# Kernel tuning notes

Hardware: AMD Instinct MI355X
Metric: run time of the kernel (lower is better)

Reference implementation:

```python
import jax, jax.numpy as jnp
import numpy as np

B, S, D, H = 4, 2048, 1024, 16
HD = D // H  # head dim = 64
NEG = jnp.finfo(jnp.float32).min


def setup_inputs() -> dict:
    key = jax.random.key(0)
    ks = jax.random.split(key, 6)
    states = jax.random.normal(ks[0], (B, S, D), dtype=jnp.float32)
    # causal float mask, broadcastable over batch and heads
    mask = jnp.tril(jnp.ones((S, S), dtype=jnp.float32))[None, None, :, :]
    scale = 1.0 / np.sqrt(D)
    Wq = jax.random.normal(ks[1], (D, D), dtype=jnp.float32) * scale
    Wk = jax.random.normal(ks[2], (D, D), dtype=jnp.float32) * scale
    Wv = jax.random.normal(ks[3], (D, D), dtype=jnp.float32) * scale
    Wo = jax.random.normal(ks[4], (D, D), dtype=jnp.float32) * scale
    return {"states": states, "mask": mask, "Wq": Wq, "Wk": Wk, "Wv": Wv, "Wo": Wo}


def _split_heads(x):
    # [B,S,D] -> [B,H,S,HD]
    return x.reshape(B, S, H, HD).transpose(0, 2, 1, 3)


def reference(states, mask, Wq, Wk, Wv, Wo):
    q = _split_heads(states @ Wq)
    k = _split_heads(states @ Wk)
    v = _split_heads(states @ Wv)
    # scores [B,H,S,S], scaled by rsqrt(head_dim) as in the original
    alpha = jnp.einsum("bhqd,bhkd->bhqk", q, k) * (1.0 / jnp.sqrt(jnp.float32(HD)))
    alpha = alpha * mask + (1.0 - mask) * NEG
    alpha = jax.nn.softmax(alpha, axis=-1)
    ctx = jnp.einsum("bhqk,bhkd->bhqd", alpha, v)
    ctx = ctx.transpose(0, 2, 1, 3).reshape(B, S, D)  # concat heads
    return ctx @ Wo
```

## Files before the change

### kernel.cpp

```cpp
#include <hip/hip_runtime.h>
#include <hip/hip_bf16.h>

#define BB 4
#define SS 2048
#define DD 1024
#define HH 16
#define HDD 64
#define MM (BB*SS)

typedef __attribute__((ext_vector_type(8))) short short8;
typedef __attribute__((ext_vector_type(4))) float f32x4;
typedef __attribute__((ext_vector_type(4))) int int4v;
typedef __attribute__((ext_vector_type(4))) short bf16x4;

__device__ __forceinline__ ushort f2bf(float f) {
  union { float f; uint u; } v; v.f = f;
  uint u = v.u;
  uint r = (u + 0x7FFFu + ((u >> 16) & 1u)) >> 16;
  return (ushort)r;
}

__device__ __forceinline__ float exp2f_fast(float x) {
#if __has_builtin(__builtin_amdgcn_exp2f)
  return __builtin_amdgcn_exp2f(x);
#else
  float r; asm("v_exp_f32 %0, %1" : "=v"(r) : "v"(x)); return r;
#endif
}

__device__ __forceinline__ bf16x4 pack4bf(float a, float b, float c, float d) {
  union { __hip_bfloat162 h2[2]; bf16x4 s; } u;
  u.h2[0] = __float22bfloat162_rn(make_float2(a, b));
  u.h2[1] = __float22bfloat162_rn(make_float2(c, d));
  return u.s;
}

__device__ __forceinline__ f32x4 mfma16(bf16x4 a, bf16x4 b, f32x4 c) {
#if __has_builtin(__builtin_amdgcn_mfma_f32_16x16x16bf16_1k)
  return __builtin_amdgcn_mfma_f32_16x16x16bf16_1k(a, b, c, 0, 0, 0);
#else
  f32x4 d;
  asm volatile("s_nop 1\n\tv_mfma_f32_16x16x16_bf16 %0, %1, %2, %3\n\ts_nop 7\n\ts_nop 3"
               : "=v"(d) : "v"(a), "v"(b), "v"(c));
  return d;
#endif
}

__device__ __forceinline__ void gload16(void* lds, const void* g) {
  __builtin_amdgcn_global_load_lds((const __attribute__((address_space(1))) void*)g,
                                   (__attribute__((address_space(3))) void*)lds, 16, 0, 0);
}

__global__ __launch_bounds__(256) void k_convert(const float* __restrict__ in,
                                                 ushort* __restrict__ out, int n4) {
  int i = blockIdx.x * 256 + threadIdx.x;
  if (i >= n4) return;
  float4 v = ((const float4*)in)[i];
  uint lo = (uint)f2bf(v.x) | ((uint)f2bf(v.y) << 16);
  uint hi = (uint)f2bf(v.z) | ((uint)f2bf(v.w) << 16);
  ((uint2*)out)[i] = make_uint2(lo, hi);
}

__global__ __launch_bounds__(256) void k_transpose(const float* __restrict__ W0, const float* __restrict__ W1,
                                                   const float* __restrict__ W2, const float* __restrict__ W3,
                                                   ushort* __restrict__ T0, ushort* __restrict__ T1,
                                                   ushort* __restrict__ T2, ushort* __restrict__ T3) {
  __shared__ float t[32][33];
  const float* W; ushort* T;
  switch (blockIdx.z) {
    case 0: W = W0; T = T0; break;
    case 1: W = W1; T = T1; break;
    case 2: W = W2; T = T2; break;
    default: W = W3; T = T3; break;
  }
  float scale = (blockIdx.z == 0) ? 0.18033688011112042f : 1.0f;
  int tx = threadIdx.x, ty = threadIdx.y;
  int x = blockIdx.x * 32 + tx;
  int y0 = blockIdx.y * 32;
#pragma unroll
  for (int j = 0; j < 32; j += 8) t[ty + j][tx] = W[(y0 + ty + j) * DD + x];
  __syncthreads();
#pragma unroll
  for (int j = 0; j < 32; j += 8)
    T[(blockIdx.x * 32 + ty + j) * DD + y0 + tx] = f2bf(t[tx][ty + j] * scale);
}

__global__ __launch_bounds__(256) void k_vtrans(const ushort* __restrict__ V,
                                                ushort* __restrict__ Vt) {
  __shared__ ushort t[64][72];
  int bh = blockIdx.y;
  int s0 = blockIdx.x * 64;
  int tid = threadIdx.x;
  int r = tid >> 3, c8 = (tid & 7) * 8;
  const ushort* vp = V + (size_t)bh * SS * HDD;
#pragma unroll
  for (int p = 0; p < 2; p++) {
    int row = r + p * 32;
    *(int4v*)&t[row][c8] = *(const int4v*)(vp + (size_t)(s0 + row) * HDD + c8);
  }
  __syncthreads();
  int hd = tid >> 2, sc = (tid & 3) * 16;
  ushort tmp[16];
#pragma unroll
  for (int j = 0; j < 16; j++) tmp[j] = t[sc + j][hd];
  ushort* op = Vt + ((size_t)bh * HDD + hd) * SS + s0 + sc;
  *(int4v*)op = *(int4v*)tmp;
  *(int4v*)(op + 8) = *(int4v*)(tmp + 8);
}

__device__ __forceinline__ void gemm_tile(const ushort* __restrict__ Arow,
                                          const ushort* __restrict__ Brow,
                                          ushort* Al, ushort* Bl,
                                          f32x4 acc[4][4]) {
  int tid = threadIdx.x;
  int lane = tid & 63, w = tid >> 6;
  int wm = w >> 1, wn = w & 1;
  int lrow = lane & 15, lgrp = lane >> 4;
#pragma unroll
  for (int i = 0; i < 4; i++)
#pragma unroll
    for (int j = 0; j < 4; j++)
#pragma unroll
      for (int r = 0; r < 4; r++) acc[i][j][r] = 0.f;

  int srow = lane >> 2;
  int scolb = (lane & 3) * 16;
  const char* A8 = (const char*)Arow;
  const char* B8 = (const char*)Brow;

#pragma unroll
  for (int ii = 0; ii < 2; ii++) {
    int i = w * 2 + ii;
    gload16(Al + i * 512, A8 + (size_t)(i * 16 + srow) * (DD * 2) + scolb);
    gload16(Bl + i * 512, B8 + (size_t)(i * 16 + srow) * (DD * 2) + scolb);
  }
  __syncthreads();

  for (int kk = 0; kk < DD; kk += 32) {
    int cur = (kk >> 5) & 1;
    if (kk + 32 < DD) {
#pragma unroll
      for (int ii = 0; ii < 2; ii++) {
        int i = w * 2 + ii;
        gload16(Al + (cur ^ 1) * 4096 + i * 512,
                A8 + (size_t)(i * 16 + srow) * (DD * 2) + (kk + 32) * 2 + scolb);
        gload16(Bl + (cur ^ 1) * 4096 + i * 512,
                B8 + (size_t)(i * 16 + srow) * (DD * 2) + (kk + 32) * 2 + scolb);
      }
    }
    short8 a[4], b[4];
#pragma unroll
    for (int i = 0; i < 4; i++) a[i] = *(const short8*)&Al[cur * 4096 + (wm * 64 + i * 16 + lrow) * 32 + lgrp * 8];
#pragma unroll
    for (int j = 0; j < 4; j++) b[j] = *(const short8*)&Bl[cur * 4096 + (wn * 64 + j * 16 + lrow) * 32 + lgrp * 8];
#pragma unroll
    for (int i = 0; i < 4; i++)
#pragma unroll
      for (int j = 0; j < 4; j++)
        acc[i][j] = __builtin_amdgcn_mfma_f32_16x16x32_bf16(a[i], b[j], acc[i][j], 0, 0, 0);
    __syncthreads();
  }
}

__global__ __launch_bounds__(256) void k_qkv(const ushort* __restrict__ X,
                                             const ushort* __restrict__ Wqt,
                                             const ushort* __restrict__ Wkt,
                                             const ushort* __restrict__ Wvt,
                                             ushort* __restrict__ Q,
                                             ushort* __restrict__ K,
                                             ushort* __restrict__ V) {
  __shared__ ushort Al[2 * 4096];
  __shared__ ushort Bl[2 * 4096];
  const ushort* Wt; ushort* Out;
  switch (blockIdx.z) {
    case 0: Wt = Wqt; Out = Q; break;
    case 1: Wt = Wkt; Out = K; break;
    default: Wt = Wvt; Out = V; break;
  }
  f32x4 acc[4][4];
  gemm_tile(X + (size_t)blockIdx.x * 128 * DD, Wt + (size_t)blockIdx.y * 128 * DD, Al, Bl, acc);
  int lane = threadIdx.x & 63, w = threadIdx.x >> 6;
  int wm = w >> 1, wn = w & 1, lrow = lane & 15, lgrp = lane >> 4;
  int m0 = blockIdx.x * 128 + wm * 64, n0 = blockIdx.y * 128 + wn * 64;
#pragma unroll
  for (int i = 0; i < 4; i++)
#pragma unroll
    for (int j = 0; j < 4; j++)
#pragma unroll
      for (int r = 0; r < 4; r++) {
        int row = m0 + i * 16 + lgrp * 4 + r;
        int col = n0 + j * 16 + lrow;
        int b = row >> 11, s = row & 2047, h = col >> 6, hd = col & 63;
        Out[(((size_t)(b * HH + h) * SS) + s) * HDD + hd] = f2bf(acc[i][j][r]);
      }
}

#define QB 128
#define KVB 64
#define NQT (SS / QB)

__global__ __launch_bounds__(256) void k_attn(const ushort* __restrict__ Q,
                                              const ushort* __restrict__ K,
                                              const ushort* __restrict__ Vt,
                                              ushort* __restrict__ Ctx) {
  __shared__ ushort Kl[2][4096];
  __shared__ ushort Vl[2][4096];
  int bh = blockIdx.y;
  int b = bh >> 4, h = bh & 15;
  int bx = blockIdx.x;
  int tid = threadIdx.x, lane = tid & 63, w = tid >> 6;
  int lrow = lane & 15, lgrp = lane >> 4;

  int srow = lane >> 3;
  int scolb = ((lane & 7) * 16) ^ (srow << 4);
  const char* K8 = (const char*)(K + (size_t)bh * SS * HDD);
  const char* V8 = (const char*)(Vt + (size_t)bh * HDD * SS);

  int kswz = (lrow & 7) << 3;
  int colE[2];
  colE[0] = (lgrp * 8) ^ kswz;
  colE[1] = (lgrp * 8 + 32) ^ kswz;

  for (int ph = 0; ph < 2; ph++) {
    int qx = ph == 0 ? (NQT - 1 - bx) : bx;
    int qb = qx * QB;
    int qw0 = qb + w * 32;
    int ntk = 2 * qx + 2;

    short8 qf[2][2];
#pragma unroll
    for (int qt = 0; qt < 2; qt++)
#pragma unroll
      for (int c = 0; c < 2; c++)
        qf[qt][c] = *(const short8*)(Q + ((size_t)bh * SS + qb + w * 32 + qt * 16 + lrow) * HDD + lgrp * 8 + 32 * c);

    f32x4 o[2][4];
#pragma unroll
    for (int qt = 0; qt < 2; qt++)
#pragma unroll
      for (int nt = 0; nt < 4; nt++)
#pragma unroll
        for (int r = 0; r < 4; r++) o[qt][nt][r] = 0.f;
    float m_run[2] = {-1e30f, -1e30f}, l_run[2] = {0.f, 0.f};

#pragma unroll
    for (int ii = 0; ii < 2; ii++) {
      int i = w + ii * 4;
      gload16(&Kl[0][i * 512], K8 + (size_t)(i * 8 + srow) * 128 + scolb);
      gload16(&Vl[0][i * 512], V8 + (size_t)(i * 8 + srow) * (SS * 2) + scolb);
    }
    __syncthreads();

    for (int kt = 0; kt < ntk; kt++) {
      int cur = kt & 1;
      if (kt + 1 < ntk) {
        int kb2 = (kt + 1) * KVB;
#pragma unroll
        for (int ii = 0; ii < 2; ii++) {
          int i = w + ii * 4;
          gload16(&Kl[cur ^ 1][i * 512], K8 + (size_t)(kb2 + i * 8 + srow) * 128 + scolb);
          gload16(&Vl[cur ^ 1][i * 512], V8 + (size_t)(i * 8 + srow) * (SS * 2) + (size_t)kb2 * 2 + scolb);
        }
      }
      int kb = kt * KVB;
      if (kb <= qw0 + 31) {
        short8 kf[4][2];
#pragma unroll
        for (int t = 0; t < 4; t++)
#pragma unroll
          for (int c = 0; c < 2; c++)
            kf[t][c] = *(const short8*)&Kl[cur][(16 * t + lrow) * 64 + colE[c]];

        bf16x4 pk[2][4];
#pragma unroll
        for (int qt = 0; qt < 2; qt++) {
          f32x4 st[4];
#pragma unroll
          for (int t = 0; t < 4; t++) {
            f32x4 z;
#pragma unroll
            for (int r = 0; r < 4; r++) z[r] = 0.f;
            z = __builtin_amdgcn_mfma_f32_16x16x32_bf16(kf[t][0], qf[qt][0], z, 0, 0, 0);
            z = __builtin_amdgcn_mfma_f32_16x16x32_bf16(kf[t][1], qf[qt][1], z, 0, 0, 0);
            st[t] = z;
          }
          if (kb + 63 > qw0) {
            int lim = qw0 + qt * 16 + lrow - kb - lgrp * 4;
#pragma unroll
            for (int t = 0; t < 4; t++)
#pragma unroll
              for (int r = 0; r < 4; r++)
                if (16 * t + r > lim) st[t][r] = -1e30f;
          }
          float rm = -1e30f;
#pragma unroll
          for (int t = 0; t < 4; t++) {
            float m01 = fmaxf(st[t][0], st[t][1]);
            float m23 = fmaxf(st[t][2], st[t][3]);
            rm = fmaxf(rm, fmaxf(m01, m23));
          }
          rm = fmaxf(rm, __shfl_xor(rm, 16));
          rm = fmaxf(rm, __shfl_xor(rm, 32));
          bool need = rm > m_run[qt] + 8.f;
          if (__any(need)) {
            float mn = need ? rm : m_run[qt];
            float sca = exp2f_fast(m_run[qt] - mn);
            m_run[qt] = mn;
            l_run[qt] *= sca;
#pragma unroll
            for (int nt = 0; nt < 4; nt++)
#pragma unroll
              for (int r = 0; r < 4; r++) o[qt][nt][r] *= sca;
          }
          float m = m_run[qt];
          float rs = 0.f;
#pragma unroll
          for (int t = 0; t < 4; t++) {
            float e0 = exp2f_fast(st[t][0] - m);
            float e1 = exp2f_fast(st[t][1] - m);
            float e2 = exp2f_fast(st[t][2] - m);
            float e3 = exp2f_fast(st[t][3] - m);
            rs += (e0 + e1) + (e2 + e3);
            pk[qt][t] = pack4bf(e0, e1, e2, e3);
          }
          rs += __shfl_xor(rs, 16);
          rs += __shfl_xor(rs, 32);
          l_run[qt] += rs;
        }

#pragma unroll
        for (int nt = 0; nt < 4; nt++) {
#pragma unroll
          for (int t = 0; t < 4; t++) {
            bf16x4 va = *(const bf16x4*)&Vl[cur][(nt * 16 + lrow) * 64 + ((16 * t + lgrp * 4) ^ kswz)];
            o[0][nt] = mfma16(va, pk[0][t], o[0][nt]);
            o[1][nt] = mfma16(va, pk[1][t], o[1][nt]);
          }
        }
      }
      __syncthreads();
    }

#pragma unroll
    for (int qt = 0; qt < 2; qt++) {
      float inv = 1.f / l_run[qt];
      int q = qb + w * 32 + qt * 16 + lrow;
      ushort* base = Ctx + ((size_t)b * SS + q) * DD + h * HDD;
#pragma unroll
      for (int nt = 0; nt < 4; nt++) {
        bf16x4 s = pack4bf(o[qt][nt][0] * inv, o[qt][nt][1] * inv,
                           o[qt][nt][2] * inv, o[qt][nt][3] * inv);
        *(bf16x4*)(base + nt * 16 + lgrp * 4) = s;
      }
    }
    __syncthreads();
  }
}

__global__ __launch_bounds__(256) void k_oproj(const ushort* __restrict__ Ctx,
                                               const ushort* __restrict__ Wot,
                                               float* __restrict__ Outp) {
  __shared__ ushort Al[2 * 4096];
  __shared__ ushort Bl[2 * 4096];
  f32x4 acc[4][4];
  gemm_tile(Ctx + (size_t)blockIdx.x * 128 * DD, Wot + (size_t)blockIdx.y * 128 * DD, Al, Bl, acc);
  int lane = threadIdx.x & 63, w = threadIdx.x >> 6;
  int wm = w >> 1, wn = w & 1, lrow = lane & 15, lgrp = lane >> 4;
  int m0 = blockIdx.x * 128 + wm * 64, n0 = blockIdx.y * 128 + wn * 64;
#pragma unroll
  for (int i = 0; i < 4; i++)
#pragma unroll
    for (int j = 0; j < 4; j++)
#pragma unroll
      for (int r = 0; r < 4; r++) {
        int row = m0 + i * 16 + lgrp * 4 + r;
        int col = n0 + j * 16 + lrow;
        Outp[(size_t)row * DD + col] = acc[i][j][r];
      }
}

extern "C" void kernel_launch(void* const* d_in, const int* in_sizes, int n_in,
                              void* d_out, int out_size, void* d_ws, size_t ws_size,
                              hipStream_t stream) {
  const float* states = (const float*)d_in[0];
  const float* Wq = (const float*)d_in[2];
  const float* Wk = (const float*)d_in[3];
  const float* Wv = (const float*)d_in[4];
  const float* Wo = (const float*)d_in[5];
  float* outp = (float*)d_out;

  char* ws = (char*)d_ws;
  const size_t XBF = 0;
  const size_t WQT = 16777216;
  const size_t WKT = WQT + 2097152;
  const size_t WVT = WKT + 2097152;
  const size_t WOT = WVT + 2097152;
  const size_t QO  = WOT + 2097152;
  const size_t KO  = QO + 16777216;
  const size_t VO  = KO + 16777216;
  const size_t CTX = VO + 16777216;

  ushort* Xbf = (ushort*)(ws + XBF);
  ushort* Wqt = (ushort*)(ws + WQT);
  ushort* Wkt = (ushort*)(ws + WKT);
  ushort* Wvt = (ushort*)(ws + WVT);
  ushort* Wot = (ushort*)(ws + WOT);
  ushort* Qb  = (ushort*)(ws + QO);
  ushort* Kb  = (ushort*)(ws + KO);
  ushort* Vb  = (ushort*)(ws + VO);
  ushort* Vtb = (ushort*)(ws + XBF);
  ushort* Ctb = (ushort*)(ws + CTX);

  k_convert<<<(MM * DD / 4 + 255) / 256, 256, 0, stream>>>(states, Xbf, MM * DD / 4);
  k_transpose<<<dim3(32, 32, 4), dim3(32, 8), 0, stream>>>(Wq, Wk, Wv, Wo, Wqt, Wkt, Wvt, Wot);
  k_qkv<<<dim3(MM / 128, DD / 128, 3), 256, 0, stream>>>(Xbf, Wqt, Wkt, Wvt, Qb, Kb, Vb);
  k_vtrans<<<dim3(SS / 64, BB * HH), 256, 0, stream>>>(Vb, Vtb);
  k_attn<<<dim3(SS / QB / 2, BB * HH), 256, 0, stream>>>(Qb, Kb, Vtb, Ctb);
  k_oproj<<<dim3(MM / 128, DD / 128), 256, 0, stream>>>(Ctb, Wot, outp);
}
```

Measured before the change: 188.4 us.

## Write V transposed from QKV GEMM and remap attention grid for XCD locality

```diff
diff --git a/kernel.cpp b/kernel.cpp
--- a/kernel.cpp
+++ b/kernel.cpp
@@ -85,29 +85,6 @@
     T[(blockIdx.x * 32 + ty + j) * DD + y0 + tx] = f2bf(t[tx][ty + j] * scale);
 }
 
-__global__ __launch_bounds__(256) void k_vtrans(const ushort* __restrict__ V,
-                                                ushort* __restrict__ Vt) {
-  __shared__ ushort t[64][72];
-  int bh = blockIdx.y;
-  int s0 = blockIdx.x * 64;
-  int tid = threadIdx.x;
-  int r = tid >> 3, c8 = (tid & 7) * 8;
-  const ushort* vp = V + (size_t)bh * SS * HDD;
-#pragma unroll
-  for (int p = 0; p < 2; p++) {
-    int row = r + p * 32;
-    *(int4v*)&t[row][c8] = *(const int4v*)(vp + (size_t)(s0 + row) * HDD + c8);
-  }
-  __syncthreads();
-  int hd = tid >> 2, sc = (tid & 3) * 16;
-  ushort tmp[16];
-#pragma unroll
-  for (int j = 0; j < 16; j++) tmp[j] = t[sc + j][hd];
-  ushort* op = Vt + ((size_t)bh * HDD + hd) * SS + s0 + sc;
-  *(int4v*)op = *(int4v*)tmp;
-  *(int4v*)(op + 8) = *(int4v*)(tmp + 8);
-}
-
 __device__ __forceinline__ void gemm_tile(const ushort* __restrict__ Arow,
                                           const ushort* __restrict__ Brow,
                                           ushort* Al, ushort* Bl,
@@ -168,31 +145,45 @@
                                              const ushort* __restrict__ Wvt,
                                              ushort* __restrict__ Q,
                                              ushort* __restrict__ K,
-                                             ushort* __restrict__ V) {
+                                             ushort* __restrict__ Vt) {
   __shared__ ushort Al[2 * 4096];
   __shared__ ushort Bl[2 * 4096];
-  const ushort* Wt; ushort* Out;
+  const ushort* Wt;
   switch (blockIdx.z) {
-    case 0: Wt = Wqt; Out = Q; break;
-    case 1: Wt = Wkt; Out = K; break;
-    default: Wt = Wvt; Out = V; break;
+    case 0: Wt = Wqt; break;
+    case 1: Wt = Wkt; break;
+    default: Wt = Wvt; break;
   }
   f32x4 acc[4][4];
   gemm_tile(X + (size_t)blockIdx.x * 128 * DD, Wt + (size_t)blockIdx.y * 128 * DD, Al, Bl, acc);
   int lane = threadIdx.x & 63, w = threadIdx.x >> 6;
   int wm = w >> 1, wn = w & 1, lrow = lane & 15, lgrp = lane >> 4;
   int m0 = blockIdx.x * 128 + wm * 64, n0 = blockIdx.y * 128 + wn * 64;
-#pragma unroll
-  for (int i = 0; i < 4; i++)
-#pragma unroll
-    for (int j = 0; j < 4; j++)
-#pragma unroll
-      for (int r = 0; r < 4; r++) {
-        int row = m0 + i * 16 + lgrp * 4 + r;
+  if (blockIdx.z == 2) {
+#pragma unroll
+    for (int i = 0; i < 4; i++)
+#pragma unroll
+      for (int j = 0; j < 4; j++) {
+        int row0 = m0 + i * 16 + lgrp * 4;
         int col = n0 + j * 16 + lrow;
-        int b = row >> 11, s = row & 2047, h = col >> 6, hd = col & 63;
-        Out[(((size_t)(b * HH + h) * SS) + s) * HDD + hd] = f2bf(acc[i][j][r]);
-      }
+        int b = row0 >> 11, s0 = row0 & 2047, h = col >> 6, hd = col & 63;
+        bf16x4 s = pack4bf(acc[i][j][0], acc[i][j][1], acc[i][j][2], acc[i][j][3]);
+        *(bf16x4*)(Vt + (((size_t)(b * HH + h) * HDD) + hd) * SS + s0) = s;
+      }
+  } else {
+    ushort* Out = (blockIdx.z == 0) ? Q : K;
+#pragma unroll
+    for (int i = 0; i < 4; i++)
+#pragma unroll
+      for (int j = 0; j < 4; j++)
+#pragma unroll
+        for (int r = 0; r < 4; r++) {
+          int row = m0 + i * 16 + lgrp * 4 + r;
+          int col = n0 + j * 16 + lrow;
+          int b = row >> 11, s = row & 2047, h = col >> 6, hd = col & 63;
+          Out[(((size_t)(b * HH + h) * SS) + s) * HDD + hd] = f2bf(acc[i][j][r]);
+        }
+  }
 }
 
 #define QB 128
@@ -205,9 +196,11 @@
                                               ushort* __restrict__ Ctx) {
   __shared__ ushort Kl[2][4096];
   __shared__ ushort Vl[2][4096];
-  int bh = blockIdx.y;
+  int bid = blockIdx.x;
+  int xcd = bid & 7, slot = bid >> 3;
+  int qx = NQT - 1 - (slot & 15);
+  int bh = (slot >> 4) * 8 + xcd;
   int b = bh >> 4, h = bh & 15;
-  int bx = blockIdx.x;
   int tid = threadIdx.x, lane = tid & 63, w = tid >> 6;
   int lrow = lane & 15, lgrp = lane >> 4;
 
@@ -221,139 +214,135 @@
   colE[0] = (lgrp * 8) ^ kswz;
   colE[1] = (lgrp * 8 + 32) ^ kswz;
 
-  for (int ph = 0; ph < 2; ph++) {
-    int qx = ph == 0 ? (NQT - 1 - bx) : bx;
-    int qb = qx * QB;
-    int qw0 = qb + w * 32;
-    int ntk = 2 * qx + 2;
-
-    short8 qf[2][2];
-#pragma unroll
-    for (int qt = 0; qt < 2; qt++)
-#pragma unroll
-      for (int c = 0; c < 2; c++)
-        qf[qt][c] = *(const short8*)(Q + ((size_t)bh * SS + qb + w * 32 + qt * 16 + lrow) * HDD + lgrp * 8 + 32 * c);
-
-    f32x4 o[2][4];
-#pragma unroll
-    for (int qt = 0; qt < 2; qt++)
-#pragma unroll
-      for (int nt = 0; nt < 4; nt++)
-#pragma unroll
-        for (int r = 0; r < 4; r++) o[qt][nt][r] = 0.f;
-    float m_run[2] = {-1e30f, -1e30f}, l_run[2] = {0.f, 0.f};
-
-#pragma unroll
-    for (int ii = 0; ii < 2; ii++) {
-      int i = w + ii * 4;
-      gload16(&Kl[0][i * 512], K8 + (size_t)(i * 8 + srow) * 128 + scolb);
-      gload16(&Vl[0][i * 512], V8 + (size_t)(i * 8 + srow) * (SS * 2) + scolb);
+  int qb = qx * QB;
+  int qw0 = qb + w * 32;
+  int ntk = 2 * qx + 2;
+
+  short8 qf[2][2];
+#pragma unroll
+  for (int qt = 0; qt < 2; qt++)
+#pragma unroll
+    for (int c = 0; c < 2; c++)
+      qf[qt][c] = *(const short8*)(Q + ((size_t)bh * SS + qb + w * 32 + qt * 16 + lrow) * HDD + lgrp * 8 + 32 * c);
+
+  f32x4 o[2][4];
+#pragma unroll
+  for (int qt = 0; qt < 2; qt++)
+#pragma unroll
+    for (int nt = 0; nt < 4; nt++)
+#pragma unroll
+      for (int r = 0; r < 4; r++) o[qt][nt][r] = 0.f;
+  float m_run[2] = {-1e30f, -1e30f}, l_run[2] = {0.f, 0.f};
+
+#pragma unroll
+  for (int ii = 0; ii < 2; ii++) {
+    int i = w + ii * 4;
+    gload16(&Kl[0][i * 512], K8 + (size_t)(i * 8 + srow) * 128 + scolb);
+    gload16(&Vl[0][i * 512], V8 + (size_t)(i * 8 + srow) * (SS * 2) + scolb);
+  }
+  __syncthreads();
+
+  for (int kt = 0; kt < ntk; kt++) {
+    int cur = kt & 1;
+    if (kt + 1 < ntk) {
+      int kb2 = (kt + 1) * KVB;
+#pragma unroll
+      for (int ii = 0; ii < 2; ii++) {
+        int i = w + ii * 4;
+        gload16(&Kl[cur ^ 1][i * 512], K8 + (size_t)(kb2 + i * 8 + srow) * 128 + scolb);
+        gload16(&Vl[cur ^ 1][i * 512], V8 + (size_t)(i * 8 + srow) * (SS * 2) + (size_t)kb2 * 2 + scolb);
+      }
+    }
+    int kb = kt * KVB;
+    if (kb <= qw0 + 31) {
+      short8 kf[4][2];
+#pragma unroll
+      for (int t = 0; t < 4; t++)
+#pragma unroll
+        for (int c = 0; c < 2; c++)
+          kf[t][c] = *(const short8*)&Kl[cur][(16 * t + lrow) * 64 + colE[c]];
+
+      bf16x4 pk[2][4];
+#pragma unroll
+      for (int qt = 0; qt < 2; qt++) {
+        f32x4 st[4];
+#pragma unroll
+        for (int t = 0; t < 4; t++) {
+          f32x4 z;
+#pragma unroll
+          for (int r = 0; r < 4; r++) z[r] = 0.f;
+          z = __builtin_amdgcn_mfma_f32_16x16x32_bf16(kf[t][0], qf[qt][0], z, 0, 0, 0);
+          z = __builtin_amdgcn_mfma_f32_16x16x32_bf16(kf[t][1], qf[qt][1], z, 0, 0, 0);
+          st[t] = z;
+        }
+        if (kb + 63 > qw0) {
+          int lim = qw0 + qt * 16 + lrow - kb - lgrp * 4;
+#pragma unroll
+          for (int t = 0; t < 4; t++)
+#pragma unroll
+            for (int r = 0; r < 4; r++)
+              if (16 * t + r > lim) st[t][r] = -1e30f;
+        }
+        float rm = -1e30f;
+#pragma unroll
+        for (int t = 0; t < 4; t++) {
+          float m01 = fmaxf(st[t][0], st[t][1]);
+          float m23 = fmaxf(st[t][2], st[t][3]);
+          rm = fmaxf(rm, fmaxf(m01, m23));
+        }
+        rm = fmaxf(rm, __shfl_xor(rm, 16));
+        rm = fmaxf(rm, __shfl_xor(rm, 32));
+        bool need = rm > m_run[qt] + 8.f;
+        if (__any(need)) {
+          float mn = need ? rm : m_run[qt];
+          float sca = exp2f_fast(m_run[qt] - mn);
+          m_run[qt] = mn;
+          l_run[qt] *= sca;
+#pragma unroll
+          for (int nt = 0; nt < 4; nt++)
+#pragma unroll
+            for (int r = 0; r < 4; r++) o[qt][nt][r] *= sca;
+        }
+        float m = m_run[qt];
+        float rs = 0.f;
+#pragma unroll
+        for (int t = 0; t < 4; t++) {
+          float e0 = exp2f_fast(st[t][0] - m);
+          float e1 = exp2f_fast(st[t][1] - m);
+          float e2 = exp2f_fast(st[t][2] - m);
+          float e3 = exp2f_fast(st[t][3] - m);
+          rs += (e0 + e1) + (e2 + e3);
+          pk[qt][t] = pack4bf(e0, e1, e2, e3);
+        }
+        rs += __shfl_xor(rs, 16);
+        rs += __shfl_xor(rs, 32);
+        l_run[qt] += rs;
+      }
+
+#pragma unroll
+      for (int nt = 0; nt < 4; nt++) {
+#pragma unroll
+        for (int t = 0; t < 4; t++) {
+          bf16x4 va = *(const bf16x4*)&Vl[cur][(nt * 16 + lrow) * 64 + ((16 * t + lgrp * 4) ^ kswz)];
+          o[0][nt] = mfma16(va, pk[0][t], o[0][nt]);
+          o[1][nt] = mfma16(va, pk[1][t], o[1][nt]);
+        }
+      }
     }
     __syncthreads();
-
-    for (int kt = 0; kt < ntk; kt++) {
-      int cur = kt & 1;
-      if (kt + 1 < ntk) {
-        int kb2 = (kt + 1) * KVB;
-#pragma unroll
-        for (int ii = 0; ii < 2; ii++) {
-          int i = w + ii * 4;
-          gload16(&Kl[cur ^ 1][i * 512], K8 + (size_t)(kb2 + i * 8 + srow) * 128 + scolb);
-          gload16(&Vl[cur ^ 1][i * 512], V8 + (size_t)(i * 8 + srow) * (SS * 2) + (size_t)kb2 * 2 + scolb);
-        }
-      }
-      int kb = kt * KVB;
-      if (kb <= qw0 + 31) {
-        short8 kf[4][2];
-#pragma unroll
-        for (int t = 0; t < 4; t++)
-#pragma unroll
-          for (int c = 0; c < 2; c++)
-            kf[t][c] = *(const short8*)&Kl[cur][(16 * t + lrow) * 64 + colE[c]];
-
-        bf16x4 pk[2][4];
-#pragma unroll
-        for (int qt = 0; qt < 2; qt++) {
-          f32x4 st[4];
-#pragma unroll
-          for (int t = 0; t < 4; t++) {
-            f32x4 z;
-#pragma unroll
-            for (int r = 0; r < 4; r++) z[r] = 0.f;
-            z = __builtin_amdgcn_mfma_f32_16x16x32_bf16(kf[t][0], qf[qt][0], z, 0, 0, 0);
-            z = __builtin_amdgcn_mfma_f32_16x16x32_bf16(kf[t][1], qf[qt][1], z, 0, 0, 0);
-            st[t] = z;
-          }
-          if (kb + 63 > qw0) {
-            int lim = qw0 + qt * 16 + lrow - kb - lgrp * 4;
-#pragma unroll
-            for (int t = 0; t < 4; t++)
-#pragma unroll
-              for (int r = 0; r < 4; r++)
-                if (16 * t + r > lim) st[t][r] = -1e30f;
-          }
-          float rm = -1e30f;
-#pragma unroll
-          for (int t = 0; t < 4; t++) {
-            float m01 = fmaxf(st[t][0], st[t][1]);
-            float m23 = fmaxf(st[t][2], st[t][3]);
-            rm = fmaxf(rm, fmaxf(m01, m23));
-          }
-          rm = fmaxf(rm, __shfl_xor(rm, 16));
-          rm = fmaxf(rm, __shfl_xor(rm, 32));
-          bool need = rm > m_run[qt] + 8.f;
-          if (__any(need)) {
-            float mn = need ? rm : m_run[qt];
-            float sca = exp2f_fast(m_run[qt] - mn);
-            m_run[qt] = mn;
-            l_run[qt] *= sca;
-#pragma unroll
-            for (int nt = 0; nt < 4; nt++)
-#pragma unroll
-              for (int r = 0; r < 4; r++) o[qt][nt][r] *= sca;
-          }
-          float m = m_run[qt];
-          float rs = 0.f;
-#pragma unroll
-          for (int t = 0; t < 4; t++) {
-            float e0 = exp2f_fast(st[t][0] - m);
-            float e1 = exp2f_fast(st[t][1] - m);
-            float e2 = exp2f_fast(st[t][2] - m);
-            float e3 = exp2f_fast(st[t][3] - m);
-            rs += (e0 + e1) + (e2 + e3);
-            pk[qt][t] = pack4bf(e0, e1, e2, e3);
-          }
-          rs += __shfl_xor(rs, 16);
-          rs += __shfl_xor(rs, 32);
-          l_run[qt] += rs;
-        }
-
-#pragma unroll
-        for (int nt = 0; nt < 4; nt++) {
-#pragma unroll
-          for (int t = 0; t < 4; t++) {
-            bf16x4 va = *(const bf16x4*)&Vl[cur][(nt * 16 + lrow) * 64 + ((16 * t + lgrp * 4) ^ kswz)];
-            o[0][nt] = mfma16(va, pk[0][t], o[0][nt]);
-            o[1][nt] = mfma16(va, pk[1][t], o[1][nt]);
-          }
-        }
-      }
-      __syncthreads();
+  }
+
+#pragma unroll
+  for (int qt = 0; qt < 2; qt++) {
+    float inv = 1.f / l_run[qt];
+    int q = qb + w * 32 + qt * 16 + lrow;
+    ushort* base = Ctx + ((size_t)b * SS + q) * DD + h * HDD;
+#pragma unroll
+    for (int nt = 0; nt < 4; nt++) {
+      bf16x4 s = pack4bf(o[qt][nt][0] * inv, o[qt][nt][1] * inv,
+                         o[qt][nt][2] * inv, o[qt][nt][3] * inv);
+      *(bf16x4*)(base + nt * 16 + lgrp * 4) = s;
     }
-
-#pragma unroll
-    for (int qt = 0; qt < 2; qt++) {
-      float inv = 1.f / l_run[qt];
-      int q = qb + w * 32 + qt * 16 + lrow;
-      ushort* base = Ctx + ((size_t)b * SS + q) * DD + h * HDD;
-#pragma unroll
-      for (int nt = 0; nt < 4; nt++) {
-        bf16x4 s = pack4bf(o[qt][nt][0] * inv, o[qt][nt][1] * inv,
-                           o[qt][nt][2] * inv, o[qt][nt][3] * inv);
-        *(bf16x4*)(base + nt * 16 + lgrp * 4) = s;
-      }
-    }
-    __syncthreads();
   }
 }
 
@@ -397,8 +386,8 @@
   const size_t WOT = WVT + 2097152;
   const size_t QO  = WOT + 2097152;
   const size_t KO  = QO + 16777216;
-  const size_t VO  = KO + 16777216;
-  const size_t CTX = VO + 16777216;
+  const size_t VT  = KO + 16777216;
+  const size_t CTX = VT + 16777216;
 
   ushort* Xbf = (ushort*)(ws + XBF);
   ushort* Wqt = (ushort*)(ws + WQT);
@@ -407,14 +396,12 @@
   ushort* Wot = (ushort*)(ws + WOT);
   ushort* Qb  = (ushort*)(ws + QO);
   ushort* Kb  = (ushort*)(ws + KO);
-  ushort* Vb  = (ushort*)(ws + VO);
-  ushort* Vtb = (ushort*)(ws + XBF);
+  ushort* Vtb = (ushort*)(ws + VT);
   ushort* Ctb = (ushort*)(ws + CTX);
 
   k_convert<<<(MM * DD / 4 + 255) / 256, 256, 0, stream>>>(states, Xbf, MM * DD / 4);
   k_transpose<<<dim3(32, 32, 4), dim3(32, 8), 0, stream>>>(Wq, Wk, Wv, Wo, Wqt, Wkt, Wvt, Wot);
-  k_qkv<<<dim3(MM / 128, DD / 128, 3), 256, 0, stream>>>(Xbf, Wqt, Wkt, Wvt, Qb, Kb, Vb);
-  k_vtrans<<<dim3(SS / 64, BB * HH), 256, 0, stream>>>(Vb, Vtb);
-  k_attn<<<dim3(SS / QB / 2, BB * HH), 256, 0, stream>>>(Qb, Kb, Vtb, Ctb);
+  k_qkv<<<dim3(MM / 128, DD / 128, 3), 256, 0, stream>>>(Xbf, Wqt, Wkt, Wvt, Qb, Kb, Vtb);
+  k_attn<<<dim3(NQT * BB * HH), 256, 0, stream>>>(Qb, Kb, Vtb, Ctb);
   k_oproj<<<dim3(MM / 128, DD / 128), 256, 0, stream>>>(Ctb, Wot, outp);
 }
```

Measured after the change: 220.1 us. +16.8%, slower.
